# Performance work log

Hardware: AMD Instinct MI355X
Metric: run time of the kernel (lower is better)

The kernel has to match this reference:

```python
import jax, jax.numpy as jnp
import numpy as np


def lrelu(x):
    return jax.nn.leaky_relu(x, 0.1)


def mask_softmax(a, mask, axis=-1):
    # faithful to the torch version: max over ALL entries, mask applied post-exp
    a_max = jnp.max(a, axis=axis, keepdims=True)
    e = jnp.exp(a - a_max) * mask
    return e / (jnp.sum(e, axis=axis, keepdims=True) + 1e-6)


def gru_cell(x, h, w_ih, w_hh, b_ih, b_hh):
    # torch.nn.GRUCell math; weights stored as [in, 3H]
    gi = x @ w_ih + b_ih
    gh = h @ w_hh + b_hh
    ir, iz, inn = jnp.split(gi, 3, axis=-1)
    hr, hz, hn = jnp.split(gh, 3, axis=-1)
    r = jax.nn.sigmoid(ir + hr)
    z = jax.nn.sigmoid(iz + hz)
    n = jnp.tanh(inn + r * hn)
    return (1 - z) * n + z * h


def setup_inputs() -> dict:
    key = jax.random.key(0)
    B, N, M, E, H, D, K = 128, 256, 12, 256, 128, 3, 2
    AF, BF, NA, NB = 82, 6, 100, 12
    ks = iter(jax.random.split(key, 64))
    nrm = lambda shape: jax.random.normal(next(ks), shape, jnp.float32) * 0.05
    return dict(
        batch_size=B,
        vertex_mask=jnp.ones((B, N), jnp.float32),
        vertex=jax.random.randint(next(ks), (B, N), 0, NA, dtype=jnp.int32),
        edge=jax.random.randint(next(ks), (B, E), 0, NB, dtype=jnp.int32),
        atom_adj=jax.random.randint(next(ks), (B * N * M,), 0, B * N, dtype=jnp.int32),
        bond_adj=jax.random.randint(next(ks), (B * N * M,), 0, B * E, dtype=jnp.int32),
        nbs_mask=jnp.ones((B, N, M), jnp.float32),
        init_atom_features=nrm((NA, AF)),
        init_bond_features=nrm((NB, BF)),
        emb_w=nrm((AF, H)), emb_b=nrm((H,)),
        Wa_main_w=nrm((D, K, H, H)), Wa_main_b=nrm((D, K, H)),
        Wbmm_w=nrm((D, K, H)), Wbmm_b=nrm((D, K)),
        Wmain_w=nrm((D, K, H, H)), Wmain_b=nrm((D, K, H)),
        Wm2s_w=nrm((D, K * H, H)), Wm2s_b=nrm((D, H)),
        Ws2m_w=nrm((D, H, H)), Ws2m_b=nrm((D, H)),
        Wsuper_w=nrm((D, H, H)), Wsuper_b=nrm((D, H)),
        Wzm1_w=nrm((D, H, H)), Wzm1_b=nrm((D, H)),
        Wzm2_w=nrm((D, H, H)), Wzm2_b=nrm((D, H)),
        Wzs1_w=nrm((D, H, H)), Wzs1_b=nrm((D, H)),
        Wzs2_w=nrm((D, H, H)), Wzs2_b=nrm((D, H)),
        U2_w=nrm((D, H + BF, H)), U2_b=nrm((D, H)),
        U1_w=nrm((D, 2 * H, H)), U1_b=nrm((D, H)),
        gm_wih=nrm((H, 3 * H)), gm_whh=nrm((H, 3 * H)), gm_bih=nrm((3 * H,)), gm_bhh=nrm((3 * H,)),
        gs_wih=nrm((H, 3 * H)), gs_whh=nrm((H, 3 * H)), gs_bih=nrm((3 * H,)), gs_bhh=nrm((3 * H,)),
    )


def reference(batch_size, vertex_mask, vertex, edge, atom_adj, bond_adj, nbs_mask,
              init_atom_features, init_bond_features, emb_w, emb_b,
              Wa_main_w, Wa_main_b, Wbmm_w, Wbmm_b, Wmain_w, Wmain_b,
              Wm2s_w, Wm2s_b, Ws2m_w, Ws2m_b, Wsuper_w, Wsuper_b,
              Wzm1_w, Wzm1_b, Wzm2_w, Wzm2_b, Wzs1_w, Wzs1_b, Wzs2_w, Wzs2_b,
              U2_w, U2_b, U1_w, U1_b,
              gm_wih, gm_whh, gm_bih, gm_bhh, gs_wih, gs_whh, gs_bih, gs_bhh):
    B = batch_size
    N = vertex_mask.shape[1]
    M = nbs_mask.shape[2]
    H = emb_w.shape[1]
    BF = init_bond_features.shape[1]
    D, K = Wa_main_w.shape[0], Wa_main_w.shape[1]

    vertex_initial = init_atom_features[vertex]          # [B,N,AF]
    edge_initial = init_bond_features[edge]              # [B,E,BF]
    vf = lrelu(vertex_initial @ emb_w + emb_b)           # [B,N,H]
    vm = vertex_mask[:, :, None]
    sf = jnp.sum(vf * vm, axis=1, keepdims=True)         # [B,1,H] super node

    for d in range(D):
        # multi-head super-node attention (all k heads vectorized)
        a_main = jnp.tanh(jnp.einsum('bnh,khg->bkng', vf, Wa_main_w[d]) + Wa_main_b[d][None, :, None, :])
        a = jnp.einsum('bkng,kg->bkn', a_main * sf[:, None, :, :], Wbmm_w[d]) + Wbmm_b[d][None, :, None]
        attn = mask_softmax(a, vertex_mask[:, None, :])                  # [B,K,N]
        wv = jnp.einsum('bnh,khg->bkng', vf, Wmain_w[d]) + Wmain_b[d][None, :, None, :]
        m = jnp.einsum('bkn,bkng->bkg', attn, wv).reshape(B, 1, K * H)   # head-concat
        main_to_super = jnp.tanh(m @ Wm2s_w[d] + Wm2s_b[d])              # [B,1,H]

        # WLN unit: gather neighbor atom/bond features, fused MLP + masked sum
        vnei = vf.reshape(-1, H)[atom_adj].reshape(B, N, M, H)
        enei = edge_initial.reshape(-1, BF)[bond_adj].reshape(B, N, M, BF)
        nei = jnp.concatenate([vnei, enei], axis=-1)                     # [B,N,M,H+BF]
        nei_label = lrelu(nei @ U2_w[d] + U2_b[d])
        nei_label = jnp.sum(nei_label * nbs_mask[..., None], axis=-2)    # [B,N,H]
        main_self = lrelu(jnp.concatenate([vf, nei_label], axis=-1) @ U1_w[d] + U1_b[d])

        super_to_main = jnp.tanh(sf @ Ws2m_w[d] + Ws2m_b[d])
        super_self = jnp.tanh(sf @ Wsuper_w[d] + Wsuper_b[d])

        z_main = jax.nn.sigmoid(main_self @ Wzm1_w[d] + Wzm1_b[d]
                                + super_to_main @ Wzm2_w[d] + Wzm2_b[d])
        hidden_main = (1 - z_main) * main_self + z_main * super_to_main
        vf = gru_cell(hidden_main.reshape(-1, H), vf.reshape(-1, H),
                      gm_wih, gm_whh, gm_bih, gm_bhh).reshape(B, N, H)

        z_super = jax.nn.sigmoid(super_self @ Wzs1_w[d] + Wzs1_b[d]
                                 + main_to_super @ Wzs2_w[d] + Wzs2_b[d])
        hidden_super = (1 - z_super) * super_self + z_super * main_to_super
        sf = gru_cell(hidden_super.reshape(B, H), sf.reshape(B, H),
                      gs_wih, gs_whh, gs_bih, gs_bhh).reshape(B, 1, H)

    return (vf, sf)
```

## Files before the change

kernel.cpp:

```cpp
#include <hip/hip_runtime.h>

typedef unsigned short ushort_t;
typedef unsigned int uint_t;
typedef __attribute__((ext_vector_type(8))) short short8;
typedef __attribute__((ext_vector_type(4))) float f32x4;

#define B   128
#define Nv  256
#define Mn  12
#define Hd  128
#define Dd  3
#define Kk  2
#define AFd 82
#define BFd 6
#define BN  (B*Nv)

enum { EPI_NONE = 0, EPI_LRELU = 1 };

__device__ __forceinline__ float lrelu(float x) { return fmaxf(x, 0.1f * x); }
__device__ __forceinline__ float sigmoidf(float x) { return 1.f / (1.f + expf(-x)); }
__device__ __forceinline__ ushort_t f2b(float x) {
    uint_t u = __float_as_uint(x);
    return (ushort_t)((u + 0x7FFFu + ((u >> 16) & 1u)) >> 16);
}
__device__ __forceinline__ float b2f(ushort_t s) {
    return __uint_as_float(((uint_t)s) << 16);
}
__device__ __forceinline__ void b2f4(uint2 u, float* o) {
    o[0] = __uint_as_float((u.x & 0xFFFFu) << 16);
    o[1] = __uint_as_float(u.x & 0xFFFF0000u);
    o[2] = __uint_as_float((u.y & 0xFFFFu) << 16);
    o[3] = __uint_as_float(u.y & 0xFFFF0000u);
}
__device__ __forceinline__ uint_t pk2(float lo, float hi) {
    return (uint_t)f2b(lo) | ((uint_t)f2b(hi) << 16);
}
__device__ __forceinline__ float upk_lo(uint_t u) { return __uint_as_float((u & 0xFFFFu) << 16); }
__device__ __forceinline__ float upk_hi(uint_t u) { return __uint_as_float(u & 0xFFFF0000u); }

struct PrepJob {
    const float* W;
    long sliceStride;
    int K, ldw, nPerSlice, Kspan, KpadRow, kDst, total, outOff, blockStart;
};
struct PrepJobs { PrepJob j[18]; int nJobs; };

__global__ __launch_bounds__(256) void k_prep_all(PrepJobs P, ushort_t* __restrict__ WT)
{
    int bid = blockIdx.x;
    int ji = 0;
    #pragma unroll 1
    while (ji + 1 < P.nJobs && P.j[ji + 1].blockStart <= bid) ++ji;
    const PrepJob J = P.j[ji];
    const int idx = (bid - J.blockStart) * 256 + threadIdx.x;
    if (idx >= J.total) return;
    const int n = idx / J.Kspan, k = idx % J.Kspan;
    const int slice = n / J.nPerSlice, nn = n % J.nPerSlice;
    float v = (k < J.K) ? J.W[(size_t)slice * J.sliceStride + (size_t)k * J.ldw + nn] : 0.f;
    WT[(size_t)J.outOff + (size_t)n * J.KpadRow + J.kDst + k] = f2b(v);
}

__global__ __launch_bounds__(256) void k_qtab(const float* __restrict__ init_bond,
                                              const float* __restrict__ U2w,
                                              ushort_t* __restrict__ qt)
{
    const int d = blockIdx.x;
    const float* W = U2w + (size_t)d * (Hd + BFd) * Hd + (size_t)Hd * Hd;
    ushort_t* q = qt + (size_t)d * 12 * Hd;
    for (int idx = threadIdx.x; idx < 12 * Hd; idx += 256) {
        const int j = idx >> 7, h = idx & 127;
        float s = 0.f;
        #pragma unroll
        for (int f = 0; f < BFd; ++f) s += init_bond[j * BFd + f] * W[f * Hd + h];
        q[idx] = f2b(s);
    }
}

template<int EPI, bool ABF, bool OBF>
__global__ __launch_bounds__(256) void mgemm(
    const void* __restrict__ A1v, int lda1, int K1,
    const int* __restrict__ rowidx,
    const ushort_t* __restrict__ Wt, int Kpad,
    const float* __restrict__ b1,
    void* __restrict__ outv, long ldo)
{
    const int t    = threadIdx.x;
    const int lane = t & 63;
    const int w    = t >> 6;
    const int wm   = w >> 1, wn = w & 1;
    const int lr   = lane & 15, lg = lane >> 4;
    const int row0 = blockIdx.x * 64;

    __shared__ ushort_t As[64 * 64];

    f32x4 acc[2][4];
    #pragma unroll
    for (int i = 0; i < 2; ++i)
        #pragma unroll
        for (int j = 0; j < 4; ++j)
            acc[i][j] = (f32x4){0.f, 0.f, 0.f, 0.f};

    const int r_st = t >> 2, q4 = t & 3;
    const int grow = row0 + r_st;
    const long arow = rowidx ? (long)rowidx[grow] : (long)grow;

    const int nck = Kpad >> 6;
    for (int ck = 0; ck < nck; ++ck) {
        if (ck) __syncthreads();
        {
            const int kb = ck * 64 + q4 * 16;
            union { ushort_t us[16]; uint4 qv[2]; } tmp;
            #pragma unroll
            for (int j = 0; j < 16; ++j) {
                const int kg = kb + j;
                ushort_t v = 0;
                if (kg < K1) {
                    if (ABF) v = ((const ushort_t*)A1v)[(size_t)arow * lda1 + kg];
                    else     v = f2b(((const float*)A1v)[(size_t)arow * lda1 + kg]);
                }
                tmp.us[j] = v;
            }
            #pragma unroll
            for (int j = 0; j < 2; ++j) {
                int byte = r_st * 128 + q4 * 32 + j * 16;
                byte ^= ((r_st & 7) << 4);
                *(uint4*)((char*)As + byte) = tmp.qv[j];
            }
        }
        __syncthreads();
        #pragma unroll
        for (int ks = 0; ks < 64; ks += 32) {
            short8 af[2], bfr[4];
            #pragma unroll
            for (int mf = 0; mf < 2; ++mf) {
                const int row = wm * 32 + mf * 16 + lr;
                int byte = row * 128 + (ks + lg * 8) * 2;
                byte ^= ((row & 7) << 4);
                af[mf] = *(const short8*)((const char*)As + byte);
            }
            #pragma unroll
            for (int nf = 0; nf < 4; ++nf) {
                const int col = wn * 64 + nf * 16 + lr;
                bfr[nf] = *(const short8*)(Wt + (size_t)col * Kpad + ck * 64 + ks + lg * 8);
            }
            #pragma unroll
            for (int mf = 0; mf < 2; ++mf)
                #pragma unroll
                for (int nf = 0; nf < 4; ++nf)
                    acc[mf][nf] = __builtin_amdgcn_mfma_f32_16x16x32_bf16(
                        af[mf], bfr[nf], acc[mf][nf], 0, 0, 0);
        }
    }

    #pragma unroll
    for (int mf = 0; mf < 2; ++mf) {
        #pragma unroll
        for (int nf = 0; nf < 4; ++nf) {
            const int c = wn * 64 + nf * 16 + lr;
            #pragma unroll
            for (int reg = 0; reg < 4; ++reg) {
                const int r = wm * 32 + mf * 16 + lg * 4 + reg;
                const size_t row = (size_t)row0 + r;
                float v = acc[mf][nf][reg];
                if (b1) v += b1[c];
                if constexpr (EPI == EPI_LRELU) v = lrelu(v);
                const size_t oidx = row * ldo + c;
                if (OBF) ((ushort_t*)outv)[oidx] = f2b(v);
                else     ((float*)outv)[oidx] = v;
            }
        }
    }
}

__global__ __launch_bounds__(256) void k_tdp(
    const ushort_t* __restrict__ vfb,
    const ushort_t* __restrict__ Wt,
    const float* __restrict__ waB,
    const float* __restrict__ u2B,
    const float* __restrict__ sf,
    const float* __restrict__ wbmmW,
    const float* __restrict__ wbmmB,
    float* __restrict__ a_out,
    ushort_t* __restrict__ Pout)
{
    const int t = threadIdx.x;
    const int lane = t & 63, w = t >> 6;
    const int wm = w >> 1, wn = w & 1;
    const int lr = lane & 15, lg = lane >> 4;
    const int row0 = blockIdx.x * 64;
    const int ky = blockIdx.y;
    const int b = row0 >> 8;

    __shared__ ushort_t As[64 * 128];
    __shared__ float EUs[128], EBb[128];
    __shared__ float red[64][2];

    {
        const int r_st = t >> 2, q4 = t & 3;
        const ushort_t* src = vfb + (size_t)(row0 + r_st) * Hd + q4 * 32;
        #pragma unroll
        for (int j = 0; j < 4; ++j) {
            uint4 v = ((const uint4*)src)[j];
            int byte = r_st * 256 + q4 * 64 + j * 16;
            byte ^= ((r_st & 7) << 4);
            *(uint4*)((char*)As + byte) = v;
        }
    }
    if (ky != 2 && t < 128) {
        EUs[t] = sf[b * Hd + t] * wbmmW[ky * Hd + t];
        EBb[t] = waB[ky * Hd + t];
    }
    __syncthreads();

    const ushort_t* Wty = Wt + (size_t)ky * 16384;

    f32x4 acc[2][4];
    #pragma unroll
    for (int i = 0; i < 2; ++i)
        #pragma unroll
        for (int j = 0; j < 4; ++j)
            acc[i][j] = (f32x4){0.f, 0.f, 0.f, 0.f};

    #pragma unroll
    for (int kk = 0; kk < 128; kk += 32) {
        short8 af[2], bfr[4];
        #pragma unroll
        for (int nf = 0; nf < 4; ++nf) {
            const int col = wn * 64 + nf * 16 + lr;
            bfr[nf] = *(const short8*)(Wty + (size_t)col * 128 + kk + lg * 8);
        }
        #pragma unroll
        for (int mf = 0; mf < 2; ++mf) {
            const int row = wm * 32 + mf * 16 + lr;
            int byte = row * 256 + (kk + lg * 8) * 2;
            byte ^= ((row & 7) << 4);
            af[mf] = *(const short8*)((const char*)As + byte);
        }
        #pragma unroll
        for (int mf = 0; mf < 2; ++mf)
            #pragma unroll
            for (int nf = 0; nf < 4; ++nf)
                acc[mf][nf] = __builtin_amdgcn_mfma_f32_16x16x32_bf16(
                    af[mf], bfr[nf], acc[mf][nf], 0, 0, 0);
    }

    if (ky == 2) {
        #pragma unroll
        for (int mf = 0; mf < 2; ++mf)
            #pragma unroll
            for (int nf = 0; nf < 4; ++nf) {
                const int c = wn * 64 + nf * 16 + lr;
                #pragma unroll
                for (int reg = 0; reg < 4; ++reg) {
                    const int r = wm * 32 + mf * 16 + lg * 4 + reg;
                    Pout[(size_t)(row0 + r) * Hd + c] = f2b(acc[mf][nf][reg] + u2B[c]);
                }
            }
    } else {
        #pragma unroll
        for (int mf = 0; mf < 2; ++mf) {
            #pragma unroll
            for (int reg = 0; reg < 4; ++reg) {
                float p = 0.f;
                #pragma unroll
                for (int nf = 0; nf < 4; ++nf) {
                    const int c = wn * 64 + nf * 16 + lr;
                    p += tanhf(acc[mf][nf][reg] + EBb[c]) * EUs[c];
                }
                p += __shfl_xor(p, 1); p += __shfl_xor(p, 2);
                p += __shfl_xor(p, 4); p += __shfl_xor(p, 8);
                if (lr == 0) red[wm * 32 + mf * 16 + lg * 4 + reg][wn] = p;
            }
        }
        __syncthreads();
        if (t < 64) {
            const int gr = row0 + t;
            a_out[(size_t)(gr >> 8) * 512 + (size_t)ky * 256 + (gr & 255)] =
                red[t][0] + red[t][1] + wbmmB[ky];
        }
    }
}

__global__ __launch_bounds__(256, 3) void k_mega(
    const ushort_t* __restrict__ vfb,
    const ushort_t* __restrict__ Pb,
    const ushort_t* __restrict__ qt,
    const int* __restrict__ aadj, const int* __restrict__ badj,
    const int* __restrict__ edge, const float* __restrict__ nmask,
    const ushort_t* __restrict__ wt_u1,
    const ushort_t* __restrict__ wt_zm1,
    const ushort_t* __restrict__ wt_rz,
    const ushort_t* __restrict__ wt_inn,
    const ushort_t* __restrict__ wt_hn,
    const float* __restrict__ u1b,
    const float* __restrict__ zm1b,
    const float* __restrict__ bih, const float* __restrict__ bhh,
    const float* __restrict__ czm2, const float* __restrict__ s2m,
    void* __restrict__ outv, const int finalFp32)
{
    const int t = threadIdx.x;
    const int lane = t & 63, w = t >> 6;
    const int wm = w >> 1, wn = w & 1;
    const int lr = lane & 15, lg = lane >> 4;
    const int row0 = blockIdx.x * 64;
    const int b = row0 >> 8;

    __shared__ ushort_t As[64 * 256];
    __shared__ ushort_t aiS[64 * Mn];
    __shared__ ushort_t eiS[64 * Mn];
    __shared__ ushort_t mkS[64 * Mn];

    for (int i = t; i < 64 * Mn; i += 256) {
        const int r = i / Mn, m = i - r * Mn;
        const long g = (long)(row0 + r) * Mn + m;
        aiS[i] = (ushort_t)aadj[g];
        eiS[i] = (ushort_t)edge[badj[g]];
        mkS[i] = f2b(nmask[g]);
    }
    {
        const int r_st = t >> 2, q4 = t & 3;
        const ushort_t* src = vfb + (size_t)(row0 + r_st) * Hd + q4 * 32;
        #pragma unroll
        for (int j = 0; j < 4; ++j) {
            uint4 v = ((const uint4*)src)[j];
            int byte = r_st * 512 + q4 * 64 + j * 16;
            byte ^= ((r_st & 7) << 4);
            *(uint4*)((char*)As + byte) = v;
        }
    }
    __syncthreads();

    #pragma unroll 1
    for (int it = 0; it < 4; ++it) {
        const int idx = it * 256 + t;
        const int r = idx >> 4, h0 = (idx & 15) * 8;
        float a8[8] = {0.f,0.f,0.f,0.f,0.f,0.f,0.f,0.f};
        #pragma unroll
        for (int m = 0; m < Mn; ++m) {
            const int ai = aiS[r * Mn + m];
            const float mk = b2f(mkS[r * Mn + m]);
            const uint4 pv = *(const uint4*)&Pb[(size_t)ai * Hd + h0];
            const uint4 qv = *(const uint4*)&qt[(size_t)eiS[r * Mn + m] * Hd + h0];
            const ushort_t* pp = (const ushort_t*)&pv;
            const ushort_t* qq = (const ushort_t*)&qv;
            #pragma unroll
            for (int e = 0; e < 8; ++e) {
                const float v = b2f(pp[e]) + b2f(qq[e]);
                a8[e] = fmaf(mk, lrelu(v), a8[e]);
            }
        }
        ushort_t o8[8];
        #pragma unroll
        for (int e = 0; e < 8; ++e) o8[e] = f2b(a8[e]);
        int byte = r * 512 + (128 + h0) * 2;
        byte ^= ((r & 7) << 4);
        *(uint4*)((char*)As + byte) = *(const uint4*)o8;
    }
    __syncthreads();

    f32x4 acc[2][4];

#define ZERO_ACC() { _Pragma("unroll") for (int i = 0; i < 2; ++i) _Pragma("unroll") for (int j = 0; j < 4; ++j) acc[i][j] = (f32x4){0.f,0.f,0.f,0.f}; }
#define GEMM_PASS(WG, KPADW, KTOT, AOFF_EXPR) { \
        ZERO_ACC(); \
        _Pragma("unroll") \
        for (int kk = 0; kk < (KTOT); kk += 32) { \
            const int acol = (AOFF_EXPR); \
            short8 af[2], bfr[4]; \
            _Pragma("unroll") \
            for (int nf = 0; nf < 4; ++nf) { \
                const int col = wn * 64 + nf * 16 + lr; \
                bfr[nf] = *(const short8*)((WG) + (size_t)col * (KPADW) + kk + lg * 8); \
            } \
            _Pragma("unroll") \
            for (int mf = 0; mf < 2; ++mf) { \
                const int row = wm * 32 + mf * 16 + lr; \
                int byte = row * 512 + (acol + lg * 8) * 2; \
                byte ^= ((row & 7) << 4); \
                af[mf] = *(const short8*)((const char*)As + byte); \
            } \
            _Pragma("unroll") \
            for (int mf = 0; mf < 2; ++mf) \
                _Pragma("unroll") \
                for (int nf = 0; nf < 4; ++nf) \
                    acc[mf][nf] = __builtin_amdgcn_mfma_f32_16x16x32_bf16(af[mf], bfr[nf], acc[mf][nf], 0, 0, 0); \
        } }

    GEMM_PASS(wt_u1, 256, 256, kk);
    uint_t msp[2][4][2];
    #pragma unroll
    for (int mf = 0; mf < 2; ++mf)
        #pragma unroll
        for (int nf = 0; nf < 4; ++nf) {
            const int c = wn * 64 + nf * 16 + lr;
            const float bb = u1b[c];
            msp[mf][nf][0] = pk2(lrelu(acc[mf][nf][0] + bb), lrelu(acc[mf][nf][1] + bb));
            msp[mf][nf][1] = pk2(lrelu(acc[mf][nf][2] + bb), lrelu(acc[mf][nf][3] + bb));
        }
    __syncthreads();
    #pragma unroll
    for (int mf = 0; mf < 2; ++mf)
        #pragma unroll
        for (int nf = 0; nf < 4; ++nf) {
            const int c = wn * 64 + nf * 16 + lr;
            #pragma unroll
            for (int reg = 0; reg < 4; ++reg) {
                const int row = wm * 32 + mf * 16 + lg * 4 + reg;
                const uint_t pk = msp[mf][nf][reg >> 1];
                const ushort_t msb = (reg & 1) ? (ushort_t)(pk >> 16) : (ushort_t)(pk & 0xFFFFu);
                int byte = row * 512 + (128 + c) * 2;
                byte ^= ((row & 7) << 4);
                *(ushort_t*)((char*)As + byte) = msb;
            }
        }
    __syncthreads();

    GEMM_PASS(wt_zm1, 128, 128, 128 + kk);
    uint_t zpk[2][4][2];
    #pragma unroll
    for (int mf = 0; mf < 2; ++mf)
        #pragma unroll
        for (int nf = 0; nf < 4; ++nf) {
            const int c = wn * 64 + nf * 16 + lr;
            const float bb = zm1b[c] + czm2[b * Hd + c];
            zpk[mf][nf][0] = pk2(sigmoidf(acc[mf][nf][0] + bb), sigmoidf(acc[mf][nf][1] + bb));
            zpk[mf][nf][1] = pk2(sigmoidf(acc[mf][nf][2] + bb), sigmoidf(acc[mf][nf][3] + bb));
        }
    __syncthreads();
    #pragma unroll
    for (int mf = 0; mf < 2; ++mf)
        #pragma unroll
        for (int nf = 0; nf < 4; ++nf) {
            const int c = wn * 64 + nf * 16 + lr;
            const float s2 = s2m[b * Hd + c];
            #pragma unroll
            for (int reg = 0; reg < 4; ++reg) {
                const int row = wm * 32 + mf * 16 + lg * 4 + reg;
                const uint_t mpk = msp[mf][nf][reg >> 1];
                const uint_t zp  = zpk[mf][nf][reg >> 1];
                const float ms = (reg & 1) ? upk_hi(mpk) : upk_lo(mpk);
                const float z  = (reg & 1) ? upk_hi(zp)  : upk_lo(zp);
                const float hid = (1.f - z) * ms + z * s2;
                int byte = row * 512 + (128 + c) * 2;
                byte ^= ((row & 7) << 4);
                *(ushort_t*)((char*)As + byte) = f2b(hid);
            }
        }
    __syncthreads();

    uint_t innp[2][4][2], hnp[2][4][2];
    GEMM_PASS(wt_inn, 128, 128, 128 + kk);
    #pragma unroll
    for (int mf = 0; mf < 2; ++mf)
        #pragma unroll
        for (int nf = 0; nf < 4; ++nf) {
            const int c = wn * 64 + nf * 16 + lr;
            const float bb = bih[256 + c];
            innp[mf][nf][0] = pk2(acc[mf][nf][0] + bb, acc[mf][nf][1] + bb);
            innp[mf][nf][1] = pk2(acc[mf][nf][2] + bb, acc[mf][nf][3] + bb);
        }
    GEMM_PASS(wt_hn, 128, 128, kk);
    #pragma unroll
    for (int mf = 0; mf < 2; ++mf)
        #pragma unroll
        for (int nf = 0; nf < 4; ++nf) {
            const int c = wn * 64 + nf * 16 + lr;
            const float bb = bhh[256 + c];
            hnp[mf][nf][0] = pk2(acc[mf][nf][0] + bb, acc[mf][nf][1] + bb);
            hnp[mf][nf][1] = pk2(acc[mf][nf][2] + bb, acc[mf][nf][3] + bb);
        }
    GEMM_PASS(wt_rz, 256, 256, (kk < 128) ? (128 + kk) : (kk - 128));
    #pragma unroll
    for (int mf = 0; mf < 2; ++mf)
        #pragma unroll
        for (int nf = 0; nf < 4; ++nf) {
            const int c = wn * 64 + nf * 16 + lr;
            const float bb = bih[c] + bhh[c];
            const float r0 = sigmoidf(acc[mf][nf][0] + bb);
            const float r1 = sigmoidf(acc[mf][nf][1] + bb);
            const float r2 = sigmoidf(acc[mf][nf][2] + bb);
            const float r3 = sigmoidf(acc[mf][nf][3] + bb);
            const float n0 = tanhf(upk_lo(innp[mf][nf][0]) + r0 * upk_lo(hnp[mf][nf][0]));
            const float n1 = tanhf(upk_hi(innp[mf][nf][0]) + r1 * upk_hi(hnp[mf][nf][0]));
            const float n2 = tanhf(upk_lo(innp[mf][nf][1]) + r2 * upk_lo(hnp[mf][nf][1]));
            const float n3 = tanhf(upk_hi(innp[mf][nf][1]) + r3 * upk_hi(hnp[mf][nf][1]));
            innp[mf][nf][0] = pk2(n0, n1);
            innp[mf][nf][1] = pk2(n2, n3);
        }
    GEMM_PASS(wt_rz + 128 * 256, 256, 256, (kk < 128) ? (128 + kk) : (kk - 128));
    #pragma unroll
    for (int mf = 0; mf < 2; ++mf)
        #pragma unroll
        for (int nf = 0; nf < 4; ++nf) {
            const int c = wn * 64 + nf * 16 + lr;
            const float bb = bih[128 + c] + bhh[128 + c];
            #pragma unroll
            for (int reg = 0; reg < 4; ++reg) {
                const int rl = wm * 32 + mf * 16 + lg * 4 + reg;
                const float z = sigmoidf(acc[mf][nf][reg] + bb);
                const uint_t np = innp[mf][nf][reg >> 1];
                const float n = (reg & 1) ? upk_hi(np) : upk_lo(np);
                int byte = rl * 512 + c * 2;
                byte ^= ((rl & 7) << 4);
                const float h = b2f(*(const ushort_t*)((const char*)As + byte));
                const float o = (1.f - z) * n + z * h;
                const size_t oidx = (size_t)(row0 + rl) * Hd + c;
                if (finalFp32) ((float*)outv)[oidx] = o;
                else           ((ushort_t*)outv)[oidx] = f2b(o);
            }
        }
#undef GEMM_PASS
#undef ZERO_ACC
}

__device__ __forceinline__ void gemv1(const float* __restrict__ W0, const float* __restrict__ x0,
                                      int ldw, int off, int K,
                                      float (*red)[8][32][4],
                                      float* __restrict__ y0, int t)
{
    const int gq = t & 31, hs = t >> 5;
    const int hn = K >> 3;
    f32x4 a0 = (f32x4){0.f,0.f,0.f,0.f};
    const float* Wp0 = W0 + off + (size_t)gq * 4;
    const int h0 = hs * hn;
    #pragma unroll 8
    for (int i = 0; i < hn; ++i) {
        const float4 w0 = *(const float4*)&Wp0[(size_t)(h0 + i) * ldw];
        const float v0 = x0[h0 + i];
        a0.x = fmaf(v0, w0.x, a0.x); a0.y = fmaf(v0, w0.y, a0.y);
        a0.z = fmaf(v0, w0.z, a0.z); a0.w = fmaf(v0, w0.w, a0.w);
    }
    *(f32x4*)&red[0][hs][gq][0] = a0;
    __syncthreads();
    if (t < 128) {
        float s0 = 0.f;
        #pragma unroll
        for (int p = 0; p < 8; ++p) s0 += red[0][p][t >> 2][t & 3];
        y0[t] = s0;
    }
    __syncthreads();
}

__device__ __forceinline__ void gemv2(const float* __restrict__ W0, const float* __restrict__ x0,
                                      const float* __restrict__ W1, const float* __restrict__ x1,
                                      int ldw, int off, int K,
                                      float (*red)[8][32][4],
                                      float* __restrict__ y0, float* __restrict__ y1, int t)
{
    const int gq = t & 31, hs = t >> 5;
    const int hn = K >> 3;
    f32x4 a0 = (f32x4){0.f,0.f,0.f,0.f}, a1 = (f32x4){0.f,0.f,0.f,0.f};
    const float* Wp0 = W0 + off + (size_t)gq * 4;
    const float* Wp1 = W1 + off + (size_t)gq * 4;
    const int h0 = hs * hn;
    #pragma unroll 4
    for (int i = 0; i < hn; ++i) {
        const float4 w0 = *(const float4*)&Wp0[(size_t)(h0 + i) * ldw];
        const float4 w1 = *(const float4*)&Wp1[(size_t)(h0 + i) * ldw];
        const float v0 = x0[h0 + i], v1 = x1[h0 + i];
        a0.x = fmaf(v0, w0.x, a0.x); a0.y = fmaf(v0, w0.y, a0.y);
        a0.z = fmaf(v0, w0.z, a0.z); a0.w = fmaf(v0, w0.w, a0.w);
        a1.x = fmaf(v1, w1.x, a1.x); a1.y = fmaf(v1, w1.y, a1.y);
        a1.z = fmaf(v1, w1.z, a1.z); a1.w = fmaf(v1, w1.w, a1.w);
    }
    *(f32x4*)&red[0][hs][gq][0] = a0;
    *(f32x4*)&red[1][hs][gq][0] = a1;
    __syncthreads();
    if (t < 128) {
        float s0 = 0.f, s1 = 0.f;
        #pragma unroll
        for (int p = 0; p < 8; ++p) {
            s0 += red[0][p][t >> 2][t & 3];
            s1 += red[1][p][t >> 2][t & 3];
        }
        y0[t] = s0; y1[t] = s1;
    }
    __syncthreads();
}

__device__ __forceinline__ void gemv3(const float* __restrict__ W0, const float* __restrict__ x0,
                                      const float* __restrict__ W1, const float* __restrict__ x1,
                                      const float* __restrict__ W2, const float* __restrict__ x2,
                                      int ldw, int off, int K,
                                      float (*red)[8][32][4],
                                      float* __restrict__ y0, float* __restrict__ y1,
                                      float* __restrict__ y2, int t)
{
    const int gq = t & 31, hs = t >> 5;
    const int hn = K >> 3;
    f32x4 a0 = (f32x4){0.f,0.f,0.f,0.f}, a1 = (f32x4){0.f,0.f,0.f,0.f}, a2 = (f32x4){0.f,0.f,0.f,0.f};
    const float* Wp0 = W0 + off + (size_t)gq * 4;
    const float* Wp1 = W1 + off + (size_t)gq * 4;
    const float* Wp2 = W2 + off + (size_t)gq * 4;
    const int h0 = hs * hn;
    #pragma unroll 4
    for (int i = 0; i < hn; ++i) {
        const float4 w0 = *(const float4*)&Wp0[(size_t)(h0 + i) * ldw];
        const float4 w1 = *(const float4*)&Wp1[(size_t)(h0 + i) * ldw];
        const float4 w2 = *(const float4*)&Wp2[(size_t)(h0 + i) * ldw];
        const float v0 = x0[h0 + i], v1 = x1[h0 + i], v2 = x2[h0 + i];
        a0.x = fmaf(v0, w0.x, a0.x); a0.y = fmaf(v0, w0.y, a0.y);
        a0.z = fmaf(v0, w0.z, a0.z); a0.w = fmaf(v0, w0.w, a0.w);
        a1.x = fmaf(v1, w1.x, a1.x); a1.y = fmaf(v1, w1.y, a1.y);
        a1.z = fmaf(v1, w1.z, a1.z); a1.w = fmaf(v1, w1.w, a1.w);
        a2.x = fmaf(v2, w2.x, a2.x); a2.y = fmaf(v2, w2.y, a2.y);
        a2.z = fmaf(v2, w2.z, a2.z); a2.w = fmaf(v2, w2.w, a2.w);
    }
    *(f32x4*)&red[0][hs][gq][0] = a0;
    *(f32x4*)&red[1][hs][gq][0] = a1;
    *(f32x4*)&red[2][hs][gq][0] = a2;
    __syncthreads();
    if (t < 128) {
        float s0 = 0.f, s1 = 0.f, s2 = 0.f;
        #pragma unroll
        for (int p = 0; p < 8; ++p) {
            s0 += red[0][p][t >> 2][t & 3];
            s1 += red[1][p][t >> 2][t & 3];
            s2 += red[2][p][t >> 2][t & 3];
        }
        y0[t] = s0; y1[t] = s1; y2[t] = s2;
    }
    __syncthreads();
}

__global__ __launch_bounds__(256) void k_super(
    const float* __restrict__ a_buf, const float* __restrict__ vmask,
    const ushort_t* __restrict__ vfb,
    const float* __restrict__ sf_in,
    const float* __restrict__ Wm, const float* __restrict__ bm,
    const float* __restrict__ Wm2s, const float* __restrict__ bm2s,
    const float* __restrict__ Ws2m, const float* __restrict__ bs2m,
    const float* __restrict__ Wsup, const float* __restrict__ bsup,
    const float* __restrict__ Wzm2, const float* __restrict__ bzm2,
    const float* __restrict__ Wzs1, const float* __restrict__ bzs1,
    const float* __restrict__ Wzs2, const float* __restrict__ bzs2,
    const float* __restrict__ gwih, const float* __restrict__ gwhh,
    const float* __restrict__ gbih, const float* __restrict__ gbhh,
    float* __restrict__ s2m_g, float* __restrict__ czm2_g,
    float* __restrict__ sf_out)
{
    const int b = blockIdx.x, t = threadIdx.x;
    const int wid = t >> 6, lane = t & 63;
    __shared__ float red[3][8][32][4];
    __shared__ float att0[256], att1[256];
    __shared__ float sfl[128], tbA[128], tbB[128], mv[256];
    __shared__ float ms2[128], s2ml[128], ssl[128], hsl[128];
    __shared__ float tmp1[128], tmp2[128], tmp3[128];
    __shared__ float gib[384], ghb[384];
    __shared__ float saS[2];
    __shared__ float lm[4][2], ls[4][2];

    const float v0 = a_buf[(size_t)b * 512 + t];
    const float v1 = a_buf[(size_t)b * 512 + 256 + t];
    const float vm = vmask[b * Nv + t];
    float m0 = v0, m1 = v1;
    #pragma unroll
    for (int o = 1; o < 64; o <<= 1) {
        m0 = fmaxf(m0, __shfl_xor(m0, o));
        m1 = fmaxf(m1, __shfl_xor(m1, o));
    }
    if (lane == 0) { lm[wid][0] = m0; lm[wid][1] = m1; }
    __syncthreads();
    m0 = fmaxf(fmaxf(lm[0][0], lm[1][0]), fmaxf(lm[2][0], lm[3][0]));
    m1 = fmaxf(fmaxf(lm[0][1], lm[1][1]), fmaxf(lm[2][1], lm[3][1]));
    const float e0v = expf(v0 - m0) * vm;
    const float e1v = expf(v1 - m1) * vm;
    float s0 = e0v, s1 = e1v;
    #pragma unroll
    for (int o = 1; o < 64; o <<= 1) {
        s0 += __shfl_xor(s0, o);
        s1 += __shfl_xor(s1, o);
    }
    if (lane == 0) { ls[wid][0] = s0; ls[wid][1] = s1; }
    if (t < 128) sfl[t] = sf_in[b * Hd + t];
    __syncthreads();
    s0 = ls[0][0] + ls[1][0] + ls[2][0] + ls[3][0];
    s1 = ls[0][1] + ls[1][1] + ls[2][1] + ls[3][1];
    att0[t] = e0v / (s0 + 1e-6f);
    att1[t] = e1v / (s1 + 1e-6f);
    if (t == 0) { saS[0] = s0 / (s0 + 1e-6f); saS[1] = s1 / (s1 + 1e-6f); }
    __syncthreads();

    {
        const int hq = t & 31, ns = t >> 5;
        f32x4 a0 = (f32x4){0.f,0.f,0.f,0.f}, a1 = (f32x4){0.f,0.f,0.f,0.f};
        const ushort_t* base = vfb + (size_t)b * Nv * Hd + hq * 4;
        #pragma unroll 8
        for (int i = 0; i < 32; ++i) {
            const int n = ns * 32 + i;
            float xv[4];
            b2f4(*(const uint2*)&base[(size_t)n * Hd], xv);
            const float w0 = att0[n], w1 = att1[n];
            a0.x = fmaf(w0, xv[0], a0.x); a0.y = fmaf(w0, xv[1], a0.y);
            a0.z = fmaf(w0, xv[2], a0.z); a0.w = fmaf(w0, xv[3], a0.w);
            a1.x = fmaf(w1, xv[0], a1.x); a1.y = fmaf(w1, xv[1], a1.y);
            a1.z = fmaf(w1, xv[2], a1.z); a1.w = fmaf(w1, xv[3], a1.w);
        }
        *(f32x4*)&red[0][ns][hq][0] = a0;
        *(f32x4*)&red[1][ns][hq][0] = a1;
        __syncthreads();
        if (t < 128) {
            float u0 = 0.f, u1 = 0.f;
            #pragma unroll
            for (int p = 0; p < 8; ++p) {
                u0 += red[0][p][t >> 2][t & 3];
                u1 += red[1][p][t >> 2][t & 3];
            }
            tbA[t] = u0; tbB[t] = u1;
        }
        __syncthreads();
    }

    gemv2(Wm, tbA, Wm + Hd * Hd, tbB, Hd, 0, Hd, red, mv, mv + 128, t);
    mv[t] += saS[t >> 7] * bm[t];
    __syncthreads();

    gemv1(Wm2s, mv, Hd, 0, 2 * Hd, red, tmp1, t);
    if (t < 128) ms2[t] = tanhf(tmp1[t] + bm2s[t]);
    __syncthreads();

    gemv2(Ws2m, sfl, Wsup, sfl, Hd, 0, Hd, red, tmp1, tmp2, t);
    if (t < 128) {
        const float v = tanhf(tmp1[t] + bs2m[t]);
        s2ml[t] = v; s2m_g[b * Hd + t] = v;
        ssl[t] = tanhf(tmp2[t] + bsup[t]);
    }
    __syncthreads();

    gemv3(Wzm2, s2ml, Wzs1, ssl, Wzs2, ms2, Hd, 0, Hd, red, tmp1, tmp2, tmp3, t);
    if (t < 128) {
        czm2_g[b * Hd + t] = tmp1[t] + bzm2[t];
        const float zs = sigmoidf(tmp2[t] + bzs1[t] + tmp3[t] + bzs2[t]);
        hsl[t] = (1.f - zs) * ssl[t] + zs * ms2[t];
    }
    __syncthreads();

    #pragma unroll 1
    for (int c = 0; c < 3; ++c)
        gemv2(gwih, hsl, gwhh, sfl, 3 * Hd, c * Hd, Hd, red, gib + c * Hd, ghb + c * Hd, t);
    if (t < 128) {
        const float r = sigmoidf(gib[t] + gbih[t] + ghb[t] + gbhh[t]);
        const float z = sigmoidf(gib[128 + t] + gbih[128 + t] + ghb[128 + t] + gbhh[128 + t]);
        const float n = tanhf(gib[256 + t] + gbih[256 + t] + r * (ghb[256 + t] + gbhh[256 + t]));
        sf_out[b * Hd + t] = (1.f - z) * n + z * sfl[t];
    }
}

__global__ __launch_bounds__(256) void k_sfv(const ushort_t* __restrict__ vfb,
                                             const float* __restrict__ vmask,
                                             float* __restrict__ sf)
{
    const int b = blockIdx.x, t = threadIdx.x;
    __shared__ float vm[256];
    __shared__ float red[8][32][4];
    vm[t] = vmask[b * Nv + t];
    __syncthreads();
    const int hq = t & 31, ns = t >> 5;
    f32x4 acc = (f32x4){0.f,0.f,0.f,0.f};
    const ushort_t* base = vfb + (size_t)b * Nv * Hd + hq * 4;
    #pragma unroll 8
    for (int i = 0; i < 32; ++i) {
        const int n = ns * 32 + i;
        float xv[4];
        b2f4(*(const uint2*)&base[(size_t)n * Hd], xv);
        const float w = vm[n];
        acc.x = fmaf(w, xv[0], acc.x); acc.y = fmaf(w, xv[1], acc.y);
        acc.z = fmaf(w, xv[2], acc.z); acc.w = fmaf(w, xv[3], acc.w);
    }
    *(f32x4*)&red[ns][hq][0] = acc;
    __syncthreads();
    if (t < 128) {
        float s = 0.f;
        #pragma unroll
        for (int p = 0; p < 8; ++p) s += red[p][t >> 2][t & 3];
        sf[b * Hd + t] = s;
    }
}

extern "C" void kernel_launch(void* const* d_in, const int* in_sizes, int n_in,
                              void* d_out, int out_size, void* d_ws, size_t ws_size,
                              hipStream_t stream)
{
    (void)in_sizes; (void)n_in; (void)out_size;

    const float* vertex_mask = (const float*)d_in[1];
    const int*   vertex      = (const int*)d_in[2];
    const int*   edge        = (const int*)d_in[3];
    const int*   atom_adj    = (const int*)d_in[4];
    const int*   bond_adj    = (const int*)d_in[5];
    const float* nbs_mask    = (const float*)d_in[6];
    const float* init_atom   = (const float*)d_in[7];
    const float* init_bond   = (const float*)d_in[8];
    const float* emb_w  = (const float*)d_in[9];
    const float* emb_b  = (const float*)d_in[10];
    const float* Wa_w   = (const float*)d_in[11];
    const float* Wa_b   = (const float*)d_in[12];
    const float* Wbmm_w = (const float*)d_in[13];
    const float* Wbmm_b = (const float*)d_in[14];
    const float* Wm_w   = (const float*)d_in[15];
    const float* Wm_b   = (const float*)d_in[16];
    const float* Wm2s_w = (const float*)d_in[17];
    const float* Wm2s_b = (const float*)d_in[18];
    const float* Ws2m_w = (const float*)d_in[19];
    const float* Ws2m_b = (const float*)d_in[20];
    const float* Wsup_w = (const float*)d_in[21];
    const float* Wsup_b = (const float*)d_in[22];
    const float* Wzm1_w = (const float*)d_in[23];
    const float* Wzm1_b = (const float*)d_in[24];
    const float* Wzm2_w = (const float*)d_in[25];
    const float* Wzm2_b = (const float*)d_in[26];
    const float* Wzs1_w = (const float*)d_in[27];
    const float* Wzs1_b = (const float*)d_in[28];
    const float* Wzs2_w = (const float*)d_in[29];
    const float* Wzs2_b = (const float*)d_in[30];
    const float* U2_w   = (const float*)d_in[31];
    const float* U2_b   = (const float*)d_in[32];
    const float* U1_w   = (const float*)d_in[33];
    const float* U1_b   = (const float*)d_in[34];
    const float* gm_wih = (const float*)d_in[35];
    const float* gm_whh = (const float*)d_in[36];
    const float* gm_bih = (const float*)d_in[37];
    const float* gm_bhh = (const float*)d_in[38];
    const float* gs_wih = (const float*)d_in[39];
    const float* gs_whh = (const float*)d_in[40];
    const float* gs_bih = (const float*)d_in[41];
    const float* gs_bhh = (const float*)d_in[42];

    const size_t MB = 1u << 20;
    if (ws_size < 40 * MB) return;

    char* base = (char*)d_ws;
    ushort_t* VF0 = (ushort_t*)base;
    ushort_t* VF1 = (ushort_t*)(base + 8 * MB);
    ushort_t* Pb  = (ushort_t*)(base + 16 * MB);
    ushort_t* WT  = (ushort_t*)(base + 24 * MB);
    ushort_t* QT  = (ushort_t*)(base + 26 * MB);
    float*    S   = (float*)(base + 27 * MB);

    float* sfA    = S;
    float* sfB    = S + 16384;
    float* a_buf  = S + 32768;
    float* s2m    = S + 98304;
    float* c_zm2  = S + 114688;

    float* X1 = (float*)d_out;
    float* sf_final = X1 + (size_t)BN * Hd;

    const int OFF_EMB = 0;
    const int PERD = 98304;
    const int OFF_L0 = 16384;
    const int OFF_RZ = OFF_L0 + 3 * PERD;
    const int OFF_NH = OFF_RZ + 65536;

    PrepJobs PJ;
    int nj = 0, blk0 = 0;
    auto addJob = [&](const float* W, int K, int ldw, long sStride, int nPer,
                      int Kspan, int KpadRow, int kDst, int ncols, int outOff) {
        PrepJob& J = PJ.j[nj++];
        J.W = W; J.K = K; J.ldw = ldw; J.sliceStride = sStride; J.nPerSlice = nPer;
        J.Kspan = Kspan; J.KpadRow = KpadRow; J.kDst = kDst;
        J.total = ncols * Kspan; J.outOff = outOff; J.blockStart = blk0;
        blk0 += (J.total + 255) / 256;
    };
    addJob(emb_w, AFd, Hd, 0, Hd, 128, 128, 0, 128, OFF_EMB);
    for (int d = 0; d < Dd; ++d) {
        const int o = OFF_L0 + d * PERD;
        addJob(Wa_w + (long)d * Kk * Hd * Hd, Hd, Hd, (long)Hd * Hd, Hd, 128, 128, 0, 256, o);
        addJob(U2_w + (long)d * (Hd + BFd) * Hd, Hd, Hd, 0, Hd, 128, 128, 0, 128, o + 32768);
        addJob(U1_w + (long)d * 2 * Hd * Hd, 2 * Hd, Hd, 0, Hd, 256, 256, 0, 128, o + 49152);
        addJob(Wzm1_w + (long)d * Hd * Hd, Hd, Hd, 0, Hd, 128, 128, 0, 128, o + 81920);
    }
    addJob(gm_wih, Hd, 3 * Hd, 0, 256, 128, 256, 0,   256, OFF_RZ);
    addJob(gm_whh, Hd, 3 * Hd, 0, 256, 128, 256, 128, 256, OFF_RZ);
    addJob(gm_wih + 256, Hd, 3 * Hd, 0, 128, 128, 128, 0, 128, OFF_NH);
    addJob(gm_whh + 256, Hd, 3 * Hd, 0, 128, 128, 128, 0, 128, OFF_NH + 16384);
    PJ.nJobs = nj;
    k_prep_all<<<dim3(blk0), dim3(256), 0, stream>>>(PJ, WT);
    k_qtab<<<dim3(Dd), dim3(256), 0, stream>>>(init_bond, U2_w, QT);

    const dim3 blk(256);
    const dim3 g1(BN / 64, 1);

    mgemm<EPI_LRELU, false, true><<<g1, blk, 0, stream>>>(
        init_atom, AFd, AFd, vertex,
        WT + OFF_EMB, 128, emb_b, VF0, Hd);
    k_sfv<<<dim3(B), blk, 0, stream>>>(VF0, vertex_mask, sfA);

    for (int d = 0; d < Dd; ++d) {
        ushort_t* vin  = (d & 1) ? VF1 : VF0;
        ushort_t* vout = (d & 1) ? VF0 : VF1;
        float* sin  = (d & 1) ? sfB : sfA;
        float* sout = (d == Dd - 1) ? sf_final : ((d & 1) ? sfA : sfB);

        const int o = OFF_L0 + d * PERD;

        k_tdp<<<dim3(BN / 64, 3), blk, 0, stream>>>(
            vin, WT + o,
            Wa_b + (long)d * Kk * Hd, U2_b + (long)d * Hd,
            sin, Wbmm_w + (long)d * Kk * Hd, Wbmm_b + (long)d * Kk,
            a_buf, Pb);

        k_super<<<dim3(B), blk, 0, stream>>>(
            a_buf, vertex_mask, vin, sin,
            Wm_w + (long)d * Kk * Hd * Hd, Wm_b + (long)d * Kk * Hd,
            Wm2s_w + (long)d * Kk * Hd * Hd, Wm2s_b + (long)d * Hd,
            Ws2m_w + (long)d * Hd * Hd, Ws2m_b + (long)d * Hd,
            Wsup_w + (long)d * Hd * Hd, Wsup_b + (long)d * Hd,
            Wzm2_w + (long)d * Hd * Hd, Wzm2_b + (long)d * Hd,
            Wzs1_w + (long)d * Hd * Hd, Wzs1_b + (long)d * Hd,
            Wzs2_w + (long)d * Hd * Hd, Wzs2_b + (long)d * Hd,
            gs_wih, gs_whh, gs_bih, gs_bhh,
            s2m, c_zm2, sout);

        k_mega<<<g1, blk, 0, stream>>>(
            vin, Pb, QT + (size_t)d * 12 * Hd,
            atom_adj, bond_adj, edge, nbs_mask,
            WT + o + 49152, WT + o + 81920,
            WT + OFF_RZ, WT + OFF_NH, WT + OFF_NH + 16384,
            U1_b + (long)d * Hd, Wzm1_b + (long)d * Hd,
            gm_bih, gm_bhh,
            c_zm2, s2m,
            (d == Dd - 1) ? (void*)X1 : (void*)vout, (d == Dd - 1) ? 1 : 0);
    }
}
```

Baseline: 340.9 us.

## Split mega kernel into two 32-row kernels with global hidden buffer

The fused per-layer vertex kernel is split in two. The first handles neighbor aggregation, the U1 GEMM and the z-gate, and writes the hidden state to a global bf16 buffer. The second reloads the hidden state and vertex features and runs the GRU GEMMs. Each block now covers 32 rows with 4 waves over N, which halves the shared-memory and accumulator footprint to raise occupancy and block count. The cost is an extra kernel launch and a global write/read of the hidden tensor each layer, and the workspace layout is shifted to make room for it.

After: 355.9 us. 4.4% more time.

```diff
diff --git a/kernel.cpp b/kernel.cpp
--- a/kernel.cpp
+++ b/kernel.cpp
@@ -281,7 +281,27 @@
     }
 }
 
-__global__ __launch_bounds__(256, 3) void k_mega(
+#define ZERO_ACC2() { _Pragma("unroll") for (int i = 0; i < 2; ++i) _Pragma("unroll") for (int j = 0; j < 2; ++j) acc[i][j] = (f32x4){0.f,0.f,0.f,0.f}; }
+#define AF_L32(LC) (*(const short8*)((const char*)As + ((((mf * 16 + lr) * 512 + ((LC) + lg * 8) * 2)) ^ ((lr & 7) << 4))))
+#define GEMM_PASS32(WG, KPADW, KTOT, A_EXPR) { \
+        ZERO_ACC2(); \
+        _Pragma("unroll") \
+        for (int kk = 0; kk < (KTOT); kk += 32) { \
+            short8 af[2], bfv[2]; \
+            _Pragma("unroll") \
+            for (int nf = 0; nf < 2; ++nf) \
+                bfv[nf] = *(const short8*)((WG) + (size_t)(wn * 32 + nf * 16 + lr) * (KPADW) + kk + lg * 8); \
+            _Pragma("unroll") \
+            for (int mf = 0; mf < 2; ++mf) \
+                af[mf] = (A_EXPR); \
+            _Pragma("unroll") \
+            for (int mf = 0; mf < 2; ++mf) \
+                _Pragma("unroll") \
+                for (int nf = 0; nf < 2; ++nf) \
+                    acc[mf][nf] = __builtin_amdgcn_mfma_f32_16x16x32_bf16(af[mf], bfv[nf], acc[mf][nf], 0, 0, 0); \
+        } }
+
+__global__ __launch_bounds__(256) void k_megaA(
     const ushort_t* __restrict__ vfb,
     const ushort_t* __restrict__ Pb,
     const ushort_t* __restrict__ qt,
@@ -289,28 +309,24 @@
     const int* __restrict__ edge, const float* __restrict__ nmask,
     const ushort_t* __restrict__ wt_u1,
     const ushort_t* __restrict__ wt_zm1,
-    const ushort_t* __restrict__ wt_rz,
-    const ushort_t* __restrict__ wt_inn,
-    const ushort_t* __restrict__ wt_hn,
     const float* __restrict__ u1b,
     const float* __restrict__ zm1b,
-    const float* __restrict__ bih, const float* __restrict__ bhh,
     const float* __restrict__ czm2, const float* __restrict__ s2m,
-    void* __restrict__ outv, const int finalFp32)
+    ushort_t* __restrict__ hid_g)
 {
     const int t = threadIdx.x;
-    const int lane = t & 63, w = t >> 6;
-    const int wm = w >> 1, wn = w & 1;
+    const int lane = t & 63;
+    const int wn = t >> 6;
     const int lr = lane & 15, lg = lane >> 4;
-    const int row0 = blockIdx.x * 64;
+    const int row0 = blockIdx.x * 32;
     const int b = row0 >> 8;
 
-    __shared__ ushort_t As[64 * 256];
-    __shared__ ushort_t aiS[64 * Mn];
-    __shared__ ushort_t eiS[64 * Mn];
-    __shared__ ushort_t mkS[64 * Mn];
-
-    for (int i = t; i < 64 * Mn; i += 256) {
+    __shared__ ushort_t As[32 * 256];
+    __shared__ ushort_t aiS[32 * Mn];
+    __shared__ ushort_t eiS[32 * Mn];
+    __shared__ ushort_t mkS[32 * Mn];
+
+    for (int i = t; i < 32 * Mn; i += 256) {
         const int r = i / Mn, m = i - r * Mn;
         const long g = (long)(row0 + r) * Mn + m;
         aiS[i] = (ushort_t)aadj[g];
@@ -318,20 +334,19 @@
         mkS[i] = f2b(nmask[g]);
     }
     {
-        const int r_st = t >> 2, q4 = t & 3;
-        const ushort_t* src = vfb + (size_t)(row0 + r_st) * Hd + q4 * 32;
-        #pragma unroll
-        for (int j = 0; j < 4; ++j) {
-            uint4 v = ((const uint4*)src)[j];
-            int byte = r_st * 512 + q4 * 64 + j * 16;
-            byte ^= ((r_st & 7) << 4);
-            *(uint4*)((char*)As + byte) = v;
-        }
+        const int r_st = t >> 3, q8 = t & 7;
+        const ushort_t* src = vfb + (size_t)(row0 + r_st) * Hd + q8 * 16;
+        uint4 v0 = ((const uint4*)src)[0];
+        uint4 v1 = ((const uint4*)src)[1];
+        int byte0 = (r_st * 512 + q8 * 32)      ^ ((r_st & 7) << 4);
+        int byte1 = (r_st * 512 + q8 * 32 + 16) ^ ((r_st & 7) << 4);
+        *(uint4*)((char*)As + byte0) = v0;
+        *(uint4*)((char*)As + byte1) = v1;
     }
     __syncthreads();
 
     #pragma unroll 1
-    for (int it = 0; it < 4; ++it) {
+    for (int it = 0; it < 2; ++it) {
         const int idx = it * 256 + t;
         const int r = idx >> 4, h0 = (idx & 15) * 8;
         float a8[8] = {0.f,0.f,0.f,0.f,0.f,0.f,0.f,0.f};
@@ -358,41 +373,15 @@
     }
     __syncthreads();
 
-    f32x4 acc[2][4];
-
-#define ZERO_ACC() { _Pragma("unroll") for (int i = 0; i < 2; ++i) _Pragma("unroll") for (int j = 0; j < 4; ++j) acc[i][j] = (f32x4){0.f,0.f,0.f,0.f}; }
-#define GEMM_PASS(WG, KPADW, KTOT, AOFF_EXPR) { \
-        ZERO_ACC(); \
-        _Pragma("unroll") \
-        for (int kk = 0; kk < (KTOT); kk += 32) { \
-            const int acol = (AOFF_EXPR); \
-            short8 af[2], bfr[4]; \
-            _Pragma("unroll") \
-            for (int nf = 0; nf < 4; ++nf) { \
-                const int col = wn * 64 + nf * 16 + lr; \
-                bfr[nf] = *(const short8*)((WG) + (size_t)col * (KPADW) + kk + lg * 8); \
-            } \
-            _Pragma("unroll") \
-            for (int mf = 0; mf < 2; ++mf) { \
-                const int row = wm * 32 + mf * 16 + lr; \
-                int byte = row * 512 + (acol + lg * 8) * 2; \
-                byte ^= ((row & 7) << 4); \
-                af[mf] = *(const short8*)((const char*)As + byte); \
-            } \
-            _Pragma("unroll") \
-            for (int mf = 0; mf < 2; ++mf) \
-                _Pragma("unroll") \
-                for (int nf = 0; nf < 4; ++nf) \
-                    acc[mf][nf] = __builtin_amdgcn_mfma_f32_16x16x32_bf16(af[mf], bfr[nf], acc[mf][nf], 0, 0, 0); \
-        } }
-
-    GEMM_PASS(wt_u1, 256, 256, kk);
-    uint_t msp[2][4][2];
+    f32x4 acc[2][2];
+
+    GEMM_PASS32(wt_u1, 256, 256, AF_L32(kk));
+    uint_t msp[2][2][2];
     #pragma unroll
     for (int mf = 0; mf < 2; ++mf)
         #pragma unroll
-        for (int nf = 0; nf < 4; ++nf) {
-            const int c = wn * 64 + nf * 16 + lr;
+        for (int nf = 0; nf < 2; ++nf) {
+            const int c = wn * 32 + nf * 16 + lr;
             const float bb = u1b[c];
             msp[mf][nf][0] = pk2(lrelu(acc[mf][nf][0] + bb), lrelu(acc[mf][nf][1] + bb));
             msp[mf][nf][1] = pk2(lrelu(acc[mf][nf][2] + bb), lrelu(acc[mf][nf][3] + bb));
@@ -401,11 +390,11 @@
     #pragma unroll
     for (int mf = 0; mf < 2; ++mf)
         #pragma unroll
-        for (int nf = 0; nf < 4; ++nf) {
-            const int c = wn * 64 + nf * 16 + lr;
+        for (int nf = 0; nf < 2; ++nf) {
+            const int c = wn * 32 + nf * 16 + lr;
             #pragma unroll
             for (int reg = 0; reg < 4; ++reg) {
-                const int row = wm * 32 + mf * 16 + lg * 4 + reg;
+                const int row = mf * 16 + lg * 4 + reg;
                 const uint_t pk = msp[mf][nf][reg >> 1];
                 const ushort_t msb = (reg & 1) ? (ushort_t)(pk >> 16) : (ushort_t)(pk & 0xFFFFu);
                 int byte = row * 512 + (128 + c) * 2;
@@ -415,66 +404,90 @@
         }
     __syncthreads();
 
-    GEMM_PASS(wt_zm1, 128, 128, 128 + kk);
-    uint_t zpk[2][4][2];
+    GEMM_PASS32(wt_zm1, 128, 128, AF_L32(128 + kk));
     #pragma unroll
     for (int mf = 0; mf < 2; ++mf)
         #pragma unroll
-        for (int nf = 0; nf < 4; ++nf) {
-            const int c = wn * 64 + nf * 16 + lr;
+        for (int nf = 0; nf < 2; ++nf) {
+            const int c = wn * 32 + nf * 16 + lr;
             const float bb = zm1b[c] + czm2[b * Hd + c];
-            zpk[mf][nf][0] = pk2(sigmoidf(acc[mf][nf][0] + bb), sigmoidf(acc[mf][nf][1] + bb));
-            zpk[mf][nf][1] = pk2(sigmoidf(acc[mf][nf][2] + bb), sigmoidf(acc[mf][nf][3] + bb));
-        }
-    __syncthreads();
+            const float s2 = s2m[b * Hd + c];
+            #pragma unroll
+            for (int reg = 0; reg < 4; ++reg) {
+                const int row = mf * 16 + lg * 4 + reg;
+                const float z = sigmoidf(acc[mf][nf][reg] + bb);
+                const uint_t mpk = msp[mf][nf][reg >> 1];
+                const float ms = (reg & 1) ? upk_hi(mpk) : upk_lo(mpk);
+                hid_g[(size_t)(row0 + row) * Hd + c] = f2b((1.f - z) * ms + z * s2);
+            }
+        }
+}
+
+__global__ __launch_bounds__(256) void k_megaB(
+    const ushort_t* __restrict__ vfb,
+    const ushort_t* __restrict__ hid_g,
+    const ushort_t* __restrict__ wt_rz,
+    const ushort_t* __restrict__ wt_inn,
+    const ushort_t* __restrict__ wt_hn,
+    const float* __restrict__ bih, const float* __restrict__ bhh,
+    void* __restrict__ outv, const int finalFp32)
+{
+    const int t = threadIdx.x;
+    const int lane = t & 63;
+    const int wn = t >> 6;
+    const int lr = lane & 15, lg = lane >> 4;
+    const int row0 = blockIdx.x * 32;
+
+    __shared__ ushort_t As[32 * 256];
+
+    {
+        const int r_st = t >> 3, q8 = t & 7;
+        const ushort_t* srcH = hid_g + (size_t)(row0 + r_st) * Hd + q8 * 16;
+        const ushort_t* srcV = vfb  + (size_t)(row0 + r_st) * Hd + q8 * 16;
+        uint4 h0 = ((const uint4*)srcH)[0];
+        uint4 h1 = ((const uint4*)srcH)[1];
+        uint4 v0 = ((const uint4*)srcV)[0];
+        uint4 v1 = ((const uint4*)srcV)[1];
+        int bH0 = (r_st * 512 + q8 * 32)            ^ ((r_st & 7) << 4);
+        int bH1 = (r_st * 512 + q8 * 32 + 16)       ^ ((r_st & 7) << 4);
+        int bV0 = (r_st * 512 + 256 + q8 * 32)      ^ ((r_st & 7) << 4);
+        int bV1 = (r_st * 512 + 256 + q8 * 32 + 16) ^ ((r_st & 7) << 4);
+        *(uint4*)((char*)As + bH0) = h0;
+        *(uint4*)((char*)As + bH1) = h1;
+        *(uint4*)((char*)As + bV0) = v0;
+        *(uint4*)((char*)As + bV1) = v1;
+    }
+    __syncthreads();
+
+    f32x4 acc[2][2];
+    uint_t innp[2][2][2], hnp[2][2][2];
+
+    GEMM_PASS32(wt_inn, 128, 128, AF_L32(kk));
     #pragma unroll
     for (int mf = 0; mf < 2; ++mf)
         #pragma unroll
-        for (int nf = 0; nf < 4; ++nf) {
-            const int c = wn * 64 + nf * 16 + lr;
-            const float s2 = s2m[b * Hd + c];
-            #pragma unroll
-            for (int reg = 0; reg < 4; ++reg) {
-                const int row = wm * 32 + mf * 16 + lg * 4 + reg;
-                const uint_t mpk = msp[mf][nf][reg >> 1];
-                const uint_t zp  = zpk[mf][nf][reg >> 1];
-                const float ms = (reg & 1) ? upk_hi(mpk) : upk_lo(mpk);
-                const float z  = (reg & 1) ? upk_hi(zp)  : upk_lo(zp);
-                const float hid = (1.f - z) * ms + z * s2;
-                int byte = row * 512 + (128 + c) * 2;
-                byte ^= ((row & 7) << 4);
-                *(ushort_t*)((char*)As + byte) = f2b(hid);
-            }
-        }
-    __syncthreads();
-
-    uint_t innp[2][4][2], hnp[2][4][2];
-    GEMM_PASS(wt_inn, 128, 128, 128 + kk);
-    #pragma unroll
-    for (int mf = 0; mf < 2; ++mf)
-        #pragma unroll
-        for (int nf = 0; nf < 4; ++nf) {
-            const int c = wn * 64 + nf * 16 + lr;
+        for (int nf = 0; nf < 2; ++nf) {
+            const int c = wn * 32 + nf * 16 + lr;
             const float bb = bih[256 + c];
             innp[mf][nf][0] = pk2(acc[mf][nf][0] + bb, acc[mf][nf][1] + bb);
             innp[mf][nf][1] = pk2(acc[mf][nf][2] + bb, acc[mf][nf][3] + bb);
         }
-    GEMM_PASS(wt_hn, 128, 128, kk);
+    GEMM_PASS32(wt_hn, 128, 128, AF_L32(128 + kk));
     #pragma unroll
     for (int mf = 0; mf < 2; ++mf)
         #pragma unroll
-        for (int nf = 0; nf < 4; ++nf) {
-            const int c = wn * 64 + nf * 16 + lr;
+        for (int nf = 0; nf < 2; ++nf) {
+            const int c = wn * 32 + nf * 16 + lr;
             const float bb = bhh[256 + c];
             hnp[mf][nf][0] = pk2(acc[mf][nf][0] + bb, acc[mf][nf][1] + bb);
             hnp[mf][nf][1] = pk2(acc[mf][nf][2] + bb, acc[mf][nf][3] + bb);
         }
-    GEMM_PASS(wt_rz, 256, 256, (kk < 128) ? (128 + kk) : (kk - 128));
+    GEMM_PASS32(wt_rz, 256, 256, AF_L32(kk));
     #pragma unroll
     for (int mf = 0; mf < 2; ++mf)
         #pragma unroll
-        for (int nf = 0; nf < 4; ++nf) {
-            const int c = wn * 64 + nf * 16 + lr;
+        for (int nf = 0; nf < 2; ++nf) {
+            const int c = wn * 32 + nf * 16 + lr;
             const float bb = bih[c] + bhh[c];
             const float r0 = sigmoidf(acc[mf][nf][0] + bb);
             const float r1 = sigmoidf(acc[mf][nf][1] + bb);
@@ -487,21 +500,20 @@
             innp[mf][nf][0] = pk2(n0, n1);
             innp[mf][nf][1] = pk2(n2, n3);
         }
-    GEMM_PASS(wt_rz + 128 * 256, 256, 256, (kk < 128) ? (128 + kk) : (kk - 128));
+    GEMM_PASS32(wt_rz + 128 * 256, 256, 256, AF_L32(kk));
     #pragma unroll
     for (int mf = 0; mf < 2; ++mf)
         #pragma unroll
-        for (int nf = 0; nf < 4; ++nf) {
-            const int c = wn * 64 + nf * 16 + lr;
+        for (int nf = 0; nf < 2; ++nf) {
+            const int c = wn * 32 + nf * 16 + lr;
             const float bb = bih[128 + c] + bhh[128 + c];
             #pragma unroll
             for (int reg = 0; reg < 4; ++reg) {
-                const int rl = wm * 32 + mf * 16 + lg * 4 + reg;
+                const int rl = mf * 16 + lg * 4 + reg;
                 const float z = sigmoidf(acc[mf][nf][reg] + bb);
                 const uint_t np = innp[mf][nf][reg >> 1];
                 const float n = (reg & 1) ? upk_hi(np) : upk_lo(np);
-                int byte = rl * 512 + c * 2;
-                byte ^= ((rl & 7) << 4);
+                int byte = (rl * 512 + (128 + c) * 2) ^ ((rl & 7) << 4);
                 const float h = b2f(*(const ushort_t*)((const char*)As + byte));
                 const float o = (1.f - z) * n + z * h;
                 const size_t oidx = (size_t)(row0 + rl) * Hd + c;
@@ -509,8 +521,6 @@
                 else           ((ushort_t*)outv)[oidx] = f2b(o);
             }
         }
-#undef GEMM_PASS
-#undef ZERO_ACC
 }
 
 __device__ __forceinline__ void gemv1(const float* __restrict__ W0, const float* __restrict__ x0,
@@ -833,9 +843,10 @@
     ushort_t* VF0 = (ushort_t*)base;
     ushort_t* VF1 = (ushort_t*)(base + 8 * MB);
     ushort_t* Pb  = (ushort_t*)(base + 16 * MB);
-    ushort_t* WT  = (ushort_t*)(base + 24 * MB);
-    ushort_t* QT  = (ushort_t*)(base + 26 * MB);
-    float*    S   = (float*)(base + 27 * MB);
+    ushort_t* HID = (ushort_t*)(base + 24 * MB);
+    ushort_t* WT  = (ushort_t*)(base + 32 * MB);
+    ushort_t* QT  = (ushort_t*)(base + 34 * MB);
+    float*    S   = (float*)(base + 35 * MB);
 
     float* sfA    = S;
     float* sfB    = S + 16384;
@@ -880,6 +891,7 @@
 
     const dim3 blk(256);
     const dim3 g1(BN / 64, 1);
+    const dim3 g32(BN / 32, 1);
 
     mgemm<EPI_LRELU, false, true><<<g1, blk, 0, stream>>>(
         init_atom, AFd, AFd, vertex,
@@ -912,14 +924,17 @@
             gs_wih, gs_whh, gs_bih, gs_bhh,
             s2m, c_zm2, sout);
 
-        k_mega<<<g1, blk, 0, stream>>>(
+        k_megaA<<<g32, blk, 0, stream>>>(
             vin, Pb, QT + (size_t)d * 12 * Hd,
             atom_adj, bond_adj, edge, nbs_mask,
             WT + o + 49152, WT + o + 81920,
+            U1_b + (long)d * Hd, Wzm1_b + (long)d * Hd,
+            c_zm2, s2m, HID);
+
+        k_megaB<<<g32, blk, 0, stream>>>(
+            vin, HID,
             WT + OFF_RZ, WT + OFF_NH, WT + OFF_NH + 16384,
-            U1_b + (long)d * Hd, Wzm1_b + (long)d * Hd,
             gm_bih, gm_bhh,
-            c_zm2, s2m,
             (d == Dd - 1) ? (void*)X1 : (void*)vout, (d == Dd - 1) ? 1 : 0);
     }
 }
```
